# Optimization experiments

Measured on AMD Instinct MI355X. Metric: run time of the kernel, lower is better.

## Reference

```python
import jax, jax.numpy as jnp
import numpy as np


def setup_inputs() -> dict:
    key = jax.random.key(0)
    k1, k2, k3 = jax.random.split(key, 3)
    B, C, H, W = 16, 512, 64, 64
    K = 32
    std = 1.0 / (K * C) ** 0.5
    x = jax.random.normal(k1, (B, C, H, W), dtype=jnp.float32)
    codewords = jax.random.uniform(k2, (K, C), dtype=jnp.float32, minval=-std, maxval=std)
    scale = jax.random.uniform(k3, (K,), dtype=jnp.float32, minval=-1.0, maxval=0.0)
    return {"x": x, "codewords": codewords, "scale": scale}


def reference(x, codewords, scale):
    # x: [B, C, H, W] -> tokens [B, N, C] with N = H*W
    B, C, H, W = x.shape
    xf = x.reshape(B, C, H * W).transpose(0, 2, 1)  # [B, N, C]

    # (avoids materializing the [B, N, K, C] tensor the torch code builds)
    x_sq = jnp.sum(xf * xf, axis=-1)                 # [B, N]
    c_sq = jnp.sum(codewords * codewords, axis=-1)   # [K]
    xc = jnp.einsum('bnc,kc->bnk', xf, codewords)    # [B, N, K]
    scaled_l2 = scale * (x_sq[..., None] - 2.0 * xc + c_sq)  # [B, N, K]

    w = jax.nn.softmax(scaled_l2, axis=2)            # [B, N, K]

    # aggregate: sum_n w[b,n,k] * (x[b,n,:] - c[k,:])
    #          = einsum(w, x) - (sum_n w) * c
    enc = jnp.einsum('bnk,bnc->bkc', w, xf) - jnp.sum(w, axis=1)[..., None] * codewords
    return enc  # [B, K, C]
```

## Files before the change

### kernel.cpp

```cpp
#include <hip/hip_runtime.h>
#include <hip/hip_bf16.h>


#define B_ 16
#define C_ 512
#define N_ 4096
#define K_ 32
#define XCPAD 40

typedef __attribute__((ext_vector_type(8))) short short8;
typedef __attribute__((ext_vector_type(16))) float floatx16;

__device__ inline unsigned short f2bf(float f) {
    union { float f; unsigned u; } v; v.f = f;
    unsigned r = v.u + 0x7FFFu + ((v.u >> 16) & 1u);
    return (unsigned short)(r >> 16);
}
__device__ inline float bf2f(short s) {
    union { unsigned u; float f; } v; v.u = ((unsigned)(unsigned short)s) << 16;
    return v.f;
}

template <int USE_WS>
__global__ __launch_bounds__(256, 3)
void enc_kernel(const float* __restrict__ x, const float* __restrict__ cw,
                const float* __restrict__ scale, float* __restrict__ outp)
{
    __shared__ unsigned short XC[C_ * XCPAD];
    __shared__ float Spart[32][33];
    __shared__ unsigned short Wl[K_ * XCPAD];
    __shared__ float xsqp[4][32];
    __shared__ float csq[K_];
    __shared__ float scl[K_];
    __shared__ float wsumL[K_];

    const int tid  = threadIdx.x;
    const int wave = tid >> 6;
    const int lane = tid & 63;
    const int l31  = lane & 31;
    const int lh   = lane >> 5;

    const int b     = blockIdx.x >> 5;
    const int chunk = blockIdx.x & 31;
    const long xbase = (long)b * C_ * N_;

    if (tid < K_) scl[tid] = scale[tid];
    for (int i = tid; i < 32 * 33; i += 256) ((float*)Spart)[i] = 0.f;
    {
        const int k = tid >> 3, p = tid & 7;
        const float4* cwr = (const float4*)(cw + k * C_ + p * 64);
        float s = 0.f;
        #pragma unroll
        for (int i = 0; i < 16; ++i) {
            float4 v = cwr[i];
            s += v.x*v.x + v.y*v.y + v.z*v.z + v.w*v.w;
        }
        s += __shfl_xor(s, 1); s += __shfl_xor(s, 2); s += __shfl_xor(s, 4);
        if (p == 0) csq[k] = s;
    }

    short8 cwf[8];
    #pragma unroll
    for (int s = 0; s < 8; ++s) {
        const float* p = cw + l31 * C_ + wave * 128 + s * 16 + lh * 8;
        short8 f;
        #pragma unroll
        for (int j = 0; j < 8; ++j) f[j] = (short)f2bf(p[j]);
        cwf[s] = f;
    }

    floatx16 acc[4];
    #pragma unroll
    for (int t = 0; t < 4; ++t)
        #pragma unroll
        for (int i = 0; i < 16; ++i) acc[t][i] = 0.f;
    float wsum_r = 0.f;

    const int c0 = tid >> 3;
    const int nq = tid & 7;
    const float* xg = x + xbase + (long)c0 * N_ + chunk * 128 + nq * 4;

    float4 bufA[4], bufB[4];
    #define ISSUEQ(buf, g, q)                                            \
        { _Pragma("unroll")                                              \
          for (int j = 0; j < 4; ++j)                                    \
              buf[j] = *(const float4*)(xg + (long)(32 * ((q)*4 + j)) * N_ + (g) * 32); }

    ISSUEQ(bufA, 0, 0);
    __syncthreads();

    for (int g = 0; g < 4; ++g) {
        float sq0 = 0.f, sq1 = 0.f, sq2 = 0.f, sq3 = 0.f;
        #pragma unroll
        for (int q = 0; q < 4; ++q) {
            float4* cur = (q & 1) ? bufB : bufA;
            float4* nxt = (q & 1) ? bufA : bufB;
            if (q < 3)      { ISSUEQ(nxt, g, q + 1); }
            else if (g < 3) { ISSUEQ(nxt, g + 1, 0); }
            #pragma unroll
            for (int j = 0; j < 4; ++j) {
                const int c = c0 + 32 * (q * 4 + j);
                const float4 v = cur[j];
                sq0 += v.x*v.x; sq1 += v.y*v.y; sq2 += v.z*v.z; sq3 += v.w*v.w;
                const unsigned lo = (unsigned)f2bf(v.x) | ((unsigned)f2bf(v.y) << 16);
                const unsigned hi = (unsigned)f2bf(v.z) | ((unsigned)f2bf(v.w) << 16);
                *(uint2*)&XC[c * XCPAD + nq * 4] = make_uint2(lo, hi);
            }
        }
        #pragma unroll
        for (int m = 8; m <= 32; m <<= 1) {
            sq0 += __shfl_xor(sq0, m); sq1 += __shfl_xor(sq1, m);
            sq2 += __shfl_xor(sq2, m); sq3 += __shfl_xor(sq3, m);
        }
        if ((lane >> 3) == 0) {
            xsqp[wave][nq * 4 + 0] = sq0; xsqp[wave][nq * 4 + 1] = sq1;
            xsqp[wave][nq * 4 + 2] = sq2; xsqp[wave][nq * 4 + 3] = sq3;
        }
        __syncthreads();

        {
            floatx16 S;
            #pragma unroll
            for (int i = 0; i < 16; ++i) S[i] = 0.f;
            #pragma unroll
            for (int s = 0; s < 8; ++s) {
                const int cb = wave * 128 + s * 16 + lh * 8;
                short8 a;
                #pragma unroll
                for (int j = 0; j < 8; ++j)
                    a[j] = (short)XC[(cb + j) * XCPAD + l31];
                S = __builtin_amdgcn_mfma_f32_32x32x16_bf16(a, cwf[s], S, 0, 0, 0);
            }
            #pragma unroll
            for (int r = 0; r < 16; ++r) {
                const int n = (r & 3) + 8 * (r >> 2) + 4 * lh;
                atomicAdd(&Spart[n][l31], S[r]);
            }
        }
        __syncthreads();

        {
            const int n  = tid >> 3;
            const int kq = tid & 7;
            const float xq = xsqp[0][n] + xsqp[1][n] + xsqp[2][n] + xsqp[3][n];
            float L[4];
            #pragma unroll
            for (int i = 0; i < 4; ++i) {
                const int k = kq * 4 + i;
                const float s2 = Spart[n][k];
                Spart[n][k] = 0.f;
                L[i] = scl[k] * (xq - 2.f * s2 + csq[k]);
            }
            float m = fmaxf(fmaxf(L[0], L[1]), fmaxf(L[2], L[3]));
            m = fmaxf(m, __shfl_xor(m, 1));
            m = fmaxf(m, __shfl_xor(m, 2));
            m = fmaxf(m, __shfl_xor(m, 4));
            float e[4], sum = 0.f;
            #pragma unroll
            for (int i = 0; i < 4; ++i) { e[i] = __expf(L[i] - m); sum += e[i]; }
            sum += __shfl_xor(sum, 1); sum += __shfl_xor(sum, 2); sum += __shfl_xor(sum, 4);
            const float inv = 1.f / sum;
            #pragma unroll
            for (int i = 0; i < 4; ++i)
                Wl[(kq * 4 + i) * XCPAD + n] = f2bf(e[i] * inv);
        }
        __syncthreads();

        {
            short8 aw[2];
            #pragma unroll
            for (int sub = 0; sub < 2; ++sub)
                aw[sub] = *(const short8*)&Wl[l31 * XCPAD + sub * 16 + lh * 8];
            float ws = 0.f;
            #pragma unroll
            for (int sub = 0; sub < 2; ++sub)
                #pragma unroll
                for (int j = 0; j < 8; ++j) ws += bf2f(aw[sub][j]);
            wsum_r += ws;
            #pragma unroll
            for (int t4 = 0; t4 < 4; ++t4) {
                const int crow = (wave * 4 + t4) * 32 + l31;
                #pragma unroll
                for (int sub = 0; sub < 2; ++sub) {
                    const short8 bx = *(const short8*)&XC[crow * XCPAD + sub * 16 + lh * 8];
                    acc[t4] = __builtin_amdgcn_mfma_f32_32x32x16_bf16(aw[sub], bx, acc[t4], 0, 0, 0);
                }
            }
        }
        __syncthreads();
    }

    wsum_r += __shfl_xor(wsum_r, 32);
    if (wave == 0 && lh == 0) wsumL[l31] = wsum_r;
    __syncthreads();

    float* dst = USE_WS ? (outp + (size_t)blockIdx.x * K_ * C_)
                        : (outp + (size_t)b * K_ * C_);
    #pragma unroll
    for (int t4 = 0; t4 < 4; ++t4) {
        const int c = (wave * 4 + t4) * 32 + l31;
        #pragma unroll
        for (int r = 0; r < 16; ++r) {
            const int k = (r & 3) + 8 * (r >> 2) + 4 * lh;
            const float val = acc[t4][r] - wsumL[k] * cw[k * C_ + c];
            if (USE_WS) dst[k * C_ + c] = val;
            else        atomicAdd(dst + k * C_ + c, val);
        }
    }
}

__global__ __launch_bounds__(256)
void reduce_kernel(const float4* __restrict__ part, float4* __restrict__ out)
{
    const int gid = blockIdx.x * 256 + threadIdx.x;
    const int bb  = gid >> 12;
    const int i4  = gid & 4095;
    const float4* p = part + ((size_t)bb * 32) * 4096 + i4;
    float4 s = make_float4(0.f, 0.f, 0.f, 0.f);
    #pragma unroll
    for (int ch = 0; ch < 32; ++ch) {
        const float4 v = p[(size_t)ch * 4096];
        s.x += v.x; s.y += v.y; s.z += v.z; s.w += v.w;
    }
    out[gid] = s;
}

extern "C" void kernel_launch(void* const* d_in, const int* in_sizes, int n_in,
                              void* d_out, int out_size, void* d_ws, size_t ws_size,
                              hipStream_t stream) {
    const float* x     = (const float*)d_in[0];
    const float* cw    = (const float*)d_in[1];
    const float* scale = (const float*)d_in[2];
    float* out = (float*)d_out;

    const size_t ws_need = (size_t)512 * K_ * C_ * sizeof(float);
    if (ws_size >= ws_need) {
        float* part = (float*)d_ws;
        hipLaunchKernelGGL(enc_kernel<1>, dim3(B_ * 32), dim3(256), 0, stream,
                           x, cw, scale, part);
        hipLaunchKernelGGL(reduce_kernel, dim3(256), dim3(256), 0, stream,
                           (const float4*)part, (float4*)out);
    } else {
        hipMemsetAsync(out, 0, (size_t)out_size * sizeof(float), stream);
        hipLaunchKernelGGL(enc_kernel<0>, dim3(B_ * 32), dim3(256), 0, stream,
                           x, cw, scale, out);
    }
}
```

Baseline: 253.5 us.

## Restructure encoding kernel: per-wave token tiles, direct global loads, MFMA weight sums

New measurement: 218.4 us. 13.8% less time.

```diff
diff --git a/kernel.cpp b/kernel.cpp
--- a/kernel.cpp
+++ b/kernel.cpp
@@ -1,12 +1,12 @@
 #include <hip/hip_runtime.h>
-#include <hip/hip_bf16.h>
 
 
 #define B_ 16
 #define C_ 512
 #define N_ 4096
 #define K_ 32
-#define XCPAD 40
+#define CWS 520
+#define WLS 40
 
 typedef __attribute__((ext_vector_type(8))) short short8;
 typedef __attribute__((ext_vector_type(16))) float floatx16;
@@ -16,8 +16,8 @@
     unsigned r = v.u + 0x7FFFu + ((v.u >> 16) & 1u);
     return (unsigned short)(r >> 16);
 }
-__device__ inline float bf2f(short s) {
-    union { unsigned u; float f; } v; v.u = ((unsigned)(unsigned short)s) << 16;
+__device__ inline float bf2f(unsigned short s) {
+    union { unsigned u; float f; } v; v.u = ((unsigned)s) << 16;
     return v.f;
 }
 
@@ -26,13 +26,10 @@
 void enc_kernel(const float* __restrict__ x, const float* __restrict__ cw,
                 const float* __restrict__ scale, float* __restrict__ outp)
 {
-    __shared__ unsigned short XC[C_ * XCPAD];
-    __shared__ float Spart[32][33];
-    __shared__ unsigned short Wl[K_ * XCPAD];
-    __shared__ float xsqp[4][32];
+    __shared__ unsigned short cwT[K_ * CWS];
+    __shared__ unsigned short Wl[4][K_ * WLS];
     __shared__ float csq[K_];
     __shared__ float scl[K_];
-    __shared__ float wsumL[K_];
 
     const int tid  = threadIdx.x;
     const int wave = tid >> 6;
@@ -42,167 +39,124 @@
 
     const int b     = blockIdx.x >> 5;
     const int chunk = blockIdx.x & 31;
-    const long xbase = (long)b * C_ * N_;
+    const float* xb = x + (long)b * C_ * N_;
 
     if (tid < K_) scl[tid] = scale[tid];
-    for (int i = tid; i < 32 * 33; i += 256) ((float*)Spart)[i] = 0.f;
     {
         const int k = tid >> 3, p = tid & 7;
-        const float4* cwr = (const float4*)(cw + k * C_ + p * 64);
+        const float4* src = (const float4*)(cw + k * C_ + p * 64);
         float s = 0.f;
         #pragma unroll
         for (int i = 0; i < 16; ++i) {
-            float4 v = cwr[i];
+            const float4 v = src[i];
             s += v.x*v.x + v.y*v.y + v.z*v.z + v.w*v.w;
+            const unsigned lo = (unsigned)f2bf(v.x) | ((unsigned)f2bf(v.y) << 16);
+            const unsigned hi = (unsigned)f2bf(v.z) | ((unsigned)f2bf(v.w) << 16);
+            *(uint2*)&cwT[k * CWS + p * 64 + i * 4] = make_uint2(lo, hi);
         }
         s += __shfl_xor(s, 1); s += __shfl_xor(s, 2); s += __shfl_xor(s, 4);
         if (p == 0) csq[k] = s;
     }
-
-    short8 cwf[8];
-    #pragma unroll
-    for (int s = 0; s < 8; ++s) {
-        const float* p = cw + l31 * C_ + wave * 128 + s * 16 + lh * 8;
-        short8 f;
-        #pragma unroll
-        for (int j = 0; j < 8; ++j) f[j] = (short)f2bf(p[j]);
-        cwf[s] = f;
-    }
-
-    floatx16 acc[4];
-    #pragma unroll
-    for (int t = 0; t < 4; ++t)
-        #pragma unroll
-        for (int i = 0; i < 16; ++i) acc[t][i] = 0.f;
-    float wsum_r = 0.f;
-
-    const int c0 = tid >> 3;
-    const int nq = tid & 7;
-    const float* xg = x + xbase + (long)c0 * N_ + chunk * 128 + nq * 4;
-
-    float4 bufA[4], bufB[4];
-    #define ISSUEQ(buf, g, q)                                            \
-        { _Pragma("unroll")                                              \
-          for (int j = 0; j < 4; ++j)                                    \
-              buf[j] = *(const float4*)(xg + (long)(32 * ((q)*4 + j)) * N_ + (g) * 32); }
-
-    ISSUEQ(bufA, 0, 0);
     __syncthreads();
 
-    for (int g = 0; g < 4; ++g) {
-        float sq0 = 0.f, sq1 = 0.f, sq2 = 0.f, sq3 = 0.f;
-        #pragma unroll
-        for (int q = 0; q < 4; ++q) {
-            float4* cur = (q & 1) ? bufB : bufA;
-            float4* nxt = (q & 1) ? bufA : bufB;
-            if (q < 3)      { ISSUEQ(nxt, g, q + 1); }
-            else if (g < 3) { ISSUEQ(nxt, g + 1, 0); }
+    const int n0 = chunk * 128 + wave * 32;
+    const float* xg = xb + n0 + l31;
+
+    floatx16 S;
+    #pragma unroll
+    for (int i = 0; i < 16; ++i) S[i] = 0.f;
+    float xsq = 0.f;
+
+    #pragma unroll
+    for (int sp = 0; sp < 16; ++sp) {
+        float xv[16];
+        #pragma unroll
+        for (int u = 0; u < 16; ++u) {
+            const int c = sp * 32 + (u >> 3) * 16 + lh * 8 + (u & 7);
+            xv[u] = xg[(long)c * N_];
+        }
+        #pragma unroll
+        for (int h = 0; h < 2; ++h) {
+            const int s = sp * 2 + h;
+            const short8 af = *(const short8*)&cwT[l31 * CWS + s * 16 + lh * 8];
+            short8 bx;
             #pragma unroll
-            for (int j = 0; j < 4; ++j) {
-                const int c = c0 + 32 * (q * 4 + j);
-                const float4 v = cur[j];
-                sq0 += v.x*v.x; sq1 += v.y*v.y; sq2 += v.z*v.z; sq3 += v.w*v.w;
-                const unsigned lo = (unsigned)f2bf(v.x) | ((unsigned)f2bf(v.y) << 16);
-                const unsigned hi = (unsigned)f2bf(v.z) | ((unsigned)f2bf(v.w) << 16);
-                *(uint2*)&XC[c * XCPAD + nq * 4] = make_uint2(lo, hi);
+            for (int j = 0; j < 8; ++j) {
+                const float v = xv[h * 8 + j];
+                xsq += v * v;
+                bx[j] = (short)f2bf(v);
             }
-        }
-        #pragma unroll
-        for (int m = 8; m <= 32; m <<= 1) {
-            sq0 += __shfl_xor(sq0, m); sq1 += __shfl_xor(sq1, m);
-            sq2 += __shfl_xor(sq2, m); sq3 += __shfl_xor(sq3, m);
-        }
-        if ((lane >> 3) == 0) {
-            xsqp[wave][nq * 4 + 0] = sq0; xsqp[wave][nq * 4 + 1] = sq1;
-            xsqp[wave][nq * 4 + 2] = sq2; xsqp[wave][nq * 4 + 3] = sq3;
-        }
-        __syncthreads();
-
-        {
-            floatx16 S;
-            #pragma unroll
-            for (int i = 0; i < 16; ++i) S[i] = 0.f;
-            #pragma unroll
-            for (int s = 0; s < 8; ++s) {
-                const int cb = wave * 128 + s * 16 + lh * 8;
-                short8 a;
-                #pragma unroll
-                for (int j = 0; j < 8; ++j)
-                    a[j] = (short)XC[(cb + j) * XCPAD + l31];
-                S = __builtin_amdgcn_mfma_f32_32x32x16_bf16(a, cwf[s], S, 0, 0, 0);
-            }
-            #pragma unroll
-            for (int r = 0; r < 16; ++r) {
-                const int n = (r & 3) + 8 * (r >> 2) + 4 * lh;
-                atomicAdd(&Spart[n][l31], S[r]);
-            }
-        }
-        __syncthreads();
-
-        {
-            const int n  = tid >> 3;
-            const int kq = tid & 7;
-            const float xq = xsqp[0][n] + xsqp[1][n] + xsqp[2][n] + xsqp[3][n];
-            float L[4];
-            #pragma unroll
-            for (int i = 0; i < 4; ++i) {
-                const int k = kq * 4 + i;
-                const float s2 = Spart[n][k];
-                Spart[n][k] = 0.f;
-                L[i] = scl[k] * (xq - 2.f * s2 + csq[k]);
-            }
-            float m = fmaxf(fmaxf(L[0], L[1]), fmaxf(L[2], L[3]));
-            m = fmaxf(m, __shfl_xor(m, 1));
-            m = fmaxf(m, __shfl_xor(m, 2));
-            m = fmaxf(m, __shfl_xor(m, 4));
-            float e[4], sum = 0.f;
-            #pragma unroll
-            for (int i = 0; i < 4; ++i) { e[i] = __expf(L[i] - m); sum += e[i]; }
-            sum += __shfl_xor(sum, 1); sum += __shfl_xor(sum, 2); sum += __shfl_xor(sum, 4);
-            const float inv = 1.f / sum;
-            #pragma unroll
-            for (int i = 0; i < 4; ++i)
-                Wl[(kq * 4 + i) * XCPAD + n] = f2bf(e[i] * inv);
-        }
-        __syncthreads();
-
-        {
-            short8 aw[2];
-            #pragma unroll
-            for (int sub = 0; sub < 2; ++sub)
-                aw[sub] = *(const short8*)&Wl[l31 * XCPAD + sub * 16 + lh * 8];
-            float ws = 0.f;
-            #pragma unroll
-            for (int sub = 0; sub < 2; ++sub)
-                #pragma unroll
-                for (int j = 0; j < 8; ++j) ws += bf2f(aw[sub][j]);
-            wsum_r += ws;
-            #pragma unroll
-            for (int t4 = 0; t4 < 4; ++t4) {
-                const int crow = (wave * 4 + t4) * 32 + l31;
-                #pragma unroll
-                for (int sub = 0; sub < 2; ++sub) {
-                    const short8 bx = *(const short8*)&XC[crow * XCPAD + sub * 16 + lh * 8];
-                    acc[t4] = __builtin_amdgcn_mfma_f32_32x32x16_bf16(aw[sub], bx, acc[t4], 0, 0, 0);
-                }
-            }
-        }
-        __syncthreads();
-    }
-
-    wsum_r += __shfl_xor(wsum_r, 32);
-    if (wave == 0 && lh == 0) wsumL[l31] = wsum_r;
+            S = __builtin_amdgcn_mfma_f32_32x32x16_bf16(af, bx, S, 0, 0, 0);
+        }
+    }
+    xsq += __shfl_xor(xsq, 32);
+
+    {
+        float L[16], mx = -3.4e38f;
+        #pragma unroll
+        for (int r = 0; r < 16; ++r) {
+            const int k = (r & 3) + 8 * (r >> 2) + 4 * lh;
+            L[r] = scl[k] * (xsq - 2.f * S[r] + csq[k]);
+            mx = fmaxf(mx, L[r]);
+        }
+        mx = fmaxf(mx, __shfl_xor(mx, 32));
+        float sum = 0.f;
+        #pragma unroll
+        for (int r = 0; r < 16; ++r) { L[r] = __expf(L[r] - mx); sum += L[r]; }
+        sum += __shfl_xor(sum, 32);
+        const float inv = 1.f / sum;
+        #pragma unroll
+        for (int r = 0; r < 16; ++r) {
+            const int k = (r & 3) + 8 * (r >> 2) + 4 * lh;
+            Wl[wave][k * WLS + l31] = f2bf(L[r] * inv);
+        }
+    }
     __syncthreads();
+
+    short8 aw[8];
+    #pragma unroll
+    for (int st = 0; st < 8; ++st)
+        aw[st] = *(const short8*)&Wl[st >> 1][l31 * WLS + (st & 1) * 16 + lh * 8];
+
+    floatx16 wacc;
+    #pragma unroll
+    for (int i = 0; i < 16; ++i) wacc[i] = 0.f;
+    {
+        short8 ones;
+        #pragma unroll
+        for (int j = 0; j < 8; ++j) ones[j] = (short)0x3F80;
+        #pragma unroll
+        for (int st = 0; st < 8; ++st)
+            wacc = __builtin_amdgcn_mfma_f32_32x32x16_bf16(aw[st], ones, wacc, 0, 0, 0);
+    }
 
     float* dst = USE_WS ? (outp + (size_t)blockIdx.x * K_ * C_)
                         : (outp + (size_t)b * K_ * C_);
-    #pragma unroll
-    for (int t4 = 0; t4 < 4; ++t4) {
-        const int c = (wave * 4 + t4) * 32 + l31;
+
+    #pragma unroll
+    for (int t = 0; t < 4; ++t) {
+        const int c = wave * 128 + t * 32 + l31;
+        const float* xgc = xb + (long)c * N_ + chunk * 128 + lh * 8;
+        floatx16 acc;
+        #pragma unroll
+        for (int i = 0; i < 16; ++i) acc[i] = 0.f;
+        #pragma unroll
+        for (int st = 0; st < 8; ++st) {
+            const int noff = (st >> 1) * 32 + (st & 1) * 16;
+            const float4 v0 = *(const float4*)(xgc + noff);
+            const float4 v1 = *(const float4*)(xgc + noff + 4);
+            short8 bx;
+            bx[0] = (short)f2bf(v0.x); bx[1] = (short)f2bf(v0.y);
+            bx[2] = (short)f2bf(v0.z); bx[3] = (short)f2bf(v0.w);
+            bx[4] = (short)f2bf(v1.x); bx[5] = (short)f2bf(v1.y);
+            bx[6] = (short)f2bf(v1.z); bx[7] = (short)f2bf(v1.w);
+            acc = __builtin_amdgcn_mfma_f32_32x32x16_bf16(aw[st], bx, acc, 0, 0, 0);
+        }
         #pragma unroll
         for (int r = 0; r < 16; ++r) {
             const int k = (r & 3) + 8 * (r >> 2) + 4 * lh;
-            const float val = acc[t4][r] - wsumL[k] * cw[k * C_ + c];
+            const float cwv = bf2f(cwT[k * CWS + c]);
+            const float val = acc[r] - wacc[r] * cwv;
             if (USE_WS) dst[k * C_ + c] = val;
             else        atomicAdd(dst + k * C_ + c, val);
         }
```
